# Optimization experiments

Hardware: AMD Instinct MI355X
Metric: run time of the kernel (lower is better)

## Reference

```python
import jax, jax.numpy as jnp
import numpy as np

B, Nx, Ny = 4, 4096, 8192
M1M, M2M = 8, 8            # modes1, modes2
WID = 32                   # width
HX, HY = 64, 64            # latent grid
DIN, DOUT = 1, 1
S = 16                     # n_subdomains
G = HX * HY
EPS = 1e-6

def _cplx(w):
    return w[..., 0] + 1j * w[..., 1]

def setup_inputs():
    key = jax.random.key(0)
    ks = jax.random.split(key, 20)
    rng = np.random.default_rng(0)
    ind = np.stack([rng.permutation(Ny) for _ in range(B)]).astype(np.int32)
    sep = np.tile(np.arange(S + 1) * (Ny // S), (B, 1)).astype(np.int32)
    d = {}
    d['x'] = jax.random.normal(ks[0], (B, Nx, DIN), jnp.float32)
    d['loc'] = jax.random.uniform(ks[1], (B, Ny, 2), jnp.float32)
    d['ind'] = jnp.asarray(ind)
    d['sep'] = jnp.asarray(sep)
    def lin(k, o, i):
        s = 1.0 / np.sqrt(i)
        return jax.random.uniform(k, (o, i), jnp.float32, -s, s)
    d['W_embed1'] = lin(ks[2], G, Nx); d['b_embed1'] = jnp.zeros((G,), jnp.float32)
    d['W_embed2'] = lin(ks[3], G, Ny); d['b_embed2'] = jnp.zeros((G,), jnp.float32)
    d['W_fc0'] = lin(ks[4], WID, DIN + 2); d['b_fc0'] = jnp.zeros((WID,), jnp.float32)
    sc = 1.0 / (WID * WID)
    d['conv_w1'] = sc * jax.random.uniform(ks[5], (4, WID, WID, M1M, M2M, 2), jnp.float32)
    d['conv_w2'] = sc * jax.random.uniform(ks[6], (4, WID, WID, M1M, M2M, 2), jnp.float32)
    d['wpt'] = jax.random.normal(ks[7], (4, WID, WID), jnp.float32) / np.sqrt(WID)
    d['wpt_b'] = jnp.zeros((4, WID), jnp.float32)
    scn = 1.0 / (WID * S * DOUT)
    d['nu_w1'] = scn * jax.random.uniform(ks[8], (WID, S * DOUT, 2 * M1M + 1, M2M, 2), jnp.float32)
    d['nu_w2'] = scn * jax.random.uniform(ks[9], (WID, S * DOUT, M1M + 1, 1, 2), jnp.float32)
    scw = 1.0 / (S * DOUT)
    d['nu_w'] = scw * jax.random.uniform(ks[10], (S, DOUT), jnp.float32)
    d['nu_b'] = scw * jax.random.uniform(ks[11], (S, DOUT), jnp.float32)
    d['W_de3'] = lin(ks[12], Ny, G); d['b_de3'] = jnp.zeros((Ny,), jnp.float32)
    d['W_fc1'] = lin(ks[13], 128, WID); d['b_fc1'] = jnp.zeros((128,), jnp.float32)
    d['W_fc2'] = lin(ks[14], DOUT, 128); d['b_fc2'] = jnp.zeros((DOUT,), jnp.float32)
    return d

def _spectral_conv(x, w1, w2):
    Bc, C, H, W = x.shape
    xf = jnp.fft.rfft2(x)  # (B,C,H,W//2+1)
    of = jnp.zeros((Bc, w1.shape[1], H, W // 2 + 1), dtype=xf.dtype)
    of = of.at[:, :, :M1M, :M2M].set(jnp.einsum('bixy,ioxy->boxy', xf[:, :, :M1M, :M2M], w1))
    of = of.at[:, :, -M1M:, :M2M].set(jnp.einsum('bixy,ioxy->boxy', xf[:, :, -M1M:, :M2M], w2))
    return jnp.fft.irfft2(of, s=(H, W))

def _nu_spectral_conv(x, loc, ind, sep, nu_w1, nu_w2, nu_w, nu_b):
    Bc, C, H, W = x.shape
    Nyl = loc.shape[1]
    m1, m2 = M1M, M2M
    P1, P2 = 2 * m1 + 1, 2 * m2 + 1
    # centered FFT, padded to odd size (torch: fft2 with s=[H+1-H%2, W+1-W%2], ortho)
    ft = jnp.fft.fftshift(jnp.fft.fft2(x, s=(H + 1 - H % 2, W + 1 - W % 2), norm='ortho'), axes=(-2, -1))
    o1, o2 = ft.shape[-2] // 2, ft.shape[-1] // 2
    im1 = jnp.einsum('bixy,ioxy->boxy', ft[:, :, o1 - m1:o1 + m1 + 1, o2 - m2:o2], nu_w1)  # (B,S*O,P1,m2)
    im2 = jnp.einsum('bixy,ioxy->boxy', ft[:, :, o1 - m1:o1 + 1, o2:o2 + 1], nu_w2)[..., 0]  # (B,S*O,m1+1)
    # hermitian-symmetric image assembly (same fill order as torch code)
    images = jnp.zeros((Bc, S * DOUT, P1, P2), dtype=im1.dtype)
    images = images.at[:, :, :, :m2].set(im1)
    images = images.at[:, :, :, m2 + 1:].set(jnp.flip(im1, (-1, -2)).conj())
    col = jnp.zeros((Bc, S * DOUT, P1), dtype=im1.dtype)
    col = col.at[:, :, m1:].set(jnp.flip(im2, -1).conj())
    col = col.at[:, :, :m1 + 1].set(im2)
    col = col.at[:, :, m1].set(col[:, :, m1].real.astype(im1.dtype))
    images = images.at[:, :, :, m2].set(col).reshape(Bc, S, DOUT, P1, P2)
    # per-point subdomain id: invert (ind, sep) CSR layout
    pos_sub = jax.vmap(lambda s: jnp.searchsorted(s, jnp.arange(Nyl), side='right') - 1)(sep)
    seg = jnp.zeros((Bc, Nyl), jnp.int32).at[jnp.arange(Bc)[:, None], ind].set(pos_sub.astype(jnp.int32))
    ids = (jnp.arange(Bc)[:, None] * S + seg).reshape(-1)
    locf = loc.reshape(Bc * Nyl, 2)
    mn = jax.ops.segment_min(locf, ids, num_segments=Bc * S)[ids]
    mx = jax.ops.segment_max(locf, ids, num_segments=Bc * S)[ids]
    om = (((locf - mn) / (mx - mn + EPS)) * (2 * jnp.pi) - jnp.pi).reshape(Bc, Nyl, 2)
    # exact type-2 NUDFT (torchkbnufft convention: centered grid, ortho norm;
    # module does conj(nufft(conj(images))) => positive-sign exponent)
    n1 = jnp.arange(P1) - m1
    n2 = jnp.arange(P2) - m2
    E = jnp.exp(1j * (om[..., 0, None, None] * n1[:, None] + om[..., 1, None, None] * n2[None, :]))  # (B,Ny,P1,P2)
    vals = jnp.einsum('bsoxy,bpxy->bpso', images, E).real / np.sqrt(P1 * P2)  # (B,Ny,S,O)
    vals = jnp.take_along_axis(vals, seg[:, :, None, None], axis=2)[:, :, 0, :]  # (B,Ny,O)
    out = vals * nu_w[seg] + nu_b[seg]
    return out.transpose(0, 2, 1)  # (B,O,Ny)

def _forward(x, loc, W_embed1, b_embed1, W_embed2, b_embed2, W_fc0, b_fc0,
             conv_w1, conv_w2, wpt, wpt_b, nu_w1, nu_w2, nu_w, nu_b,
             W_de3, b_de3, W_fc1, b_fc1, W_fc2, b_fc2, ind, sep):
    Bc = x.shape[0]
    xe = jnp.einsum('bnd,gn->bgd', x, W_embed1) + b_embed1[None, :, None]
    le = jnp.einsum('bnc,gn->bgc', loc, W_embed2) + b_embed2[None, :, None]
    h = jnp.concatenate([xe, le], axis=-1).reshape(Bc, HX, HY, DIN + 2)
    h = (h @ W_fc0.T + b_fc0).transpose(0, 3, 1, 2)  # (B,width,HX,HY)
    for l in range(4):
        h1 = _spectral_conv(h, _cplx(conv_w1[l]), _cplx(conv_w2[l]))
        h2 = jnp.einsum('oc,bchw->bohw', wpt[l], h) + wpt_b[l][None, :, None, None]
        h = h1 + h2
        if l < 3:
            h = jax.nn.gelu(h, approximate=False)
    x_nu = _nu_spectral_conv(h, loc, ind, sep, _cplx(nu_w1), _cplx(nu_w2), nu_w, nu_b)  # (B,O,Ny)
    hl = h.transpose(0, 2, 3, 1)
    hl = jax.nn.gelu(hl @ W_fc1.T + b_fc1, approximate=False)
    hl = hl @ W_fc2.T + b_fc2                      # (B,HX,HY,O)
    hl = hl.reshape(Bc, G, DOUT).transpose(0, 2, 1)  # (B,O,G)
    hl = hl @ W_de3.T + b_de3                       # (B,O,Ny)
    return (hl + x_nu).transpose(0, 2, 1)           # (B,Ny,O)

def reference(x, loc, ind, sep, W_embed1, b_embed1, W_embed2, b_embed2, W_fc0, b_fc0,
              conv_w1, conv_w2, wpt, wpt_b, nu_w1, nu_w2, nu_w, nu_b,
              W_de3, b_de3, W_fc1, b_fc1, W_fc2, b_fc2):
    return _forward(x, loc, W_embed1, b_embed1, W_embed2, b_embed2, W_fc0, b_fc0,
                    conv_w1, conv_w2, wpt, wpt_b, nu_w1, nu_w2, nu_w, nu_b,
                    W_de3, b_de3, W_fc1, b_fc1, W_fc2, b_fc2, ind, sep)
```

## Files before the change

### kernel.cpp

```cpp
#include <hip/hip_runtime.h>
#include <math.h>

#define BB 4
#define NX 4096
#define NYP 8192
#define GG 4096
#define WIDTH 32
#define SS 16
#define PI_F 3.14159265358979323846f

__device__ __forceinline__ float gelu_exact(float v) {
    return 0.5f * v * (1.0f + erff(v * 0.70710678118654752f));
}

__global__ __launch_bounds__(256, 2) void k_embed(
    const float* __restrict__ x, const float* __restrict__ loc,
    const float* __restrict__ We1, const float* __restrict__ be1,
    const float* __restrict__ We2, const float* __restrict__ be2,
    const float* __restrict__ Wfc0, const float* __restrict__ bfc0,
    float* __restrict__ h0)
{
    int gbase = blockIdx.x * 8;
    int t = threadIdx.x;

    float accx[32];
    #pragma unroll
    for (int k = 0; k < 32; ++k) accx[k] = 0.f;
    for (int n4 = t; n4 < NX / 4; n4 += 256) {
        float4 xb[4];
        #pragma unroll
        for (int b = 0; b < 4; ++b)
            xb[b] = ((const float4*)(x + (size_t)b * NX))[n4];
        float4 w[8];
        #pragma unroll
        for (int r = 0; r < 8; ++r)
            w[r] = ((const float4*)(We1 + (size_t)(gbase + r) * NX))[n4];
        #pragma unroll
        for (int r = 0; r < 8; ++r)
            #pragma unroll
            for (int b = 0; b < 4; ++b)
                accx[r * 4 + b] += w[r].x * xb[b].x + w[r].y * xb[b].y
                                 + w[r].z * xb[b].z + w[r].w * xb[b].w;
    }

    float accl[64];
    #pragma unroll
    for (int k = 0; k < 64; ++k) accl[k] = 0.f;
    for (int n4 = t; n4 < NYP / 4; n4 += 256) {
        float4 p0[4], p1[4];
        #pragma unroll
        for (int b = 0; b < 4; ++b) {
            const float4* lb = (const float4*)(loc + (size_t)b * NYP * 2);
            p0[b] = lb[n4 * 2];
            p1[b] = lb[n4 * 2 + 1];
        }
        float4 w[8];
        #pragma unroll
        for (int r = 0; r < 8; ++r)
            w[r] = ((const float4*)(We2 + (size_t)(gbase + r) * NYP))[n4];
        #pragma unroll
        for (int r = 0; r < 8; ++r)
            #pragma unroll
            for (int b = 0; b < 4; ++b) {
                accl[r * 4 + b]      += w[r].x * p0[b].x + w[r].y * p0[b].z
                                      + w[r].z * p1[b].x + w[r].w * p1[b].z;
                accl[32 + r * 4 + b] += w[r].x * p0[b].y + w[r].y * p0[b].w
                                      + w[r].z * p1[b].y + w[r].w * p1[b].w;
            }
    }

    #pragma unroll
    for (int k = 0; k < 32; ++k)
        for (int off = 32; off > 0; off >>= 1) accx[k] += __shfl_down(accx[k], off);
    #pragma unroll
    for (int k = 0; k < 64; ++k)
        for (int off = 32; off > 0; off >>= 1) accl[k] += __shfl_down(accl[k], off);
    __shared__ float red[4][96];
    __shared__ float tot[96];
    int wave = t >> 6, lane = t & 63;
    if (lane == 0) {
        for (int k = 0; k < 32; ++k) red[wave][k] = accx[k];
        for (int k = 0; k < 64; ++k) red[wave][32 + k] = accl[k];
    }
    __syncthreads();
    if (t < 96) tot[t] = red[0][t] + red[1][t] + red[2][t] + red[3][t];
    __syncthreads();
    if (t < 128) {
        int b = t >> 5, w = t & 31;
        float w0 = Wfc0[w * 3 + 0], w1c = Wfc0[w * 3 + 1], w2c = Wfc0[w * 3 + 2], bb0 = bfc0[w];
        #pragma unroll
        for (int r = 0; r < 8; ++r) {
            int g = gbase + r;
            float xe = tot[r * 4 + b] + be1[g];
            float l0 = tot[32 + r * 4 + b] + be2[g];
            float l1 = tot[64 + r * 4 + b] + be2[g];
            h0[((size_t)(b * WIDTH + w)) * GG + g] = xe * w0 + l0 * w1c + l1 * w2c + bb0;
        }
    }
}

__global__ __launch_bounds__(256) void k_xf(const float* __restrict__ h, float* __restrict__ xf)
{
    int bc = blockIdx.x;
    int t = threadIdx.x;
    __shared__ float sh[64 * 66];
    __shared__ float twc[8 * 64], tws[8 * 64];
    __shared__ float s1[64 * 8 * 2];
    const float* hp = h + (size_t)bc * 4096;
    for (int i = t; i < 4096; i += 256) sh[(i >> 6) * 66 + (i & 63)] = hp[i];
    for (int i = t; i < 512; i += 256) {
        int ky = i >> 6, y = i & 63;
        float s, c;
        sincosf(-2.f * PI_F * (float)(ky * y) / 64.f, &s, &c);
        twc[i] = c; tws[i] = s;
    }
    __syncthreads();
    for (int task = t; task < 512; task += 256) {
        int xx = task >> 3, ky = task & 7;
        float sr = 0.f, si = 0.f;
        const float* row = sh + xx * 66;
        const float* tc = twc + ky * 64;
        const float* ts = tws + ky * 64;
        for (int y = 0; y < 64; ++y) { sr += row[y] * tc[y]; si += row[y] * ts[y]; }
        s1[(xx * 8 + ky) * 2 + 0] = sr;
        s1[(xx * 8 + ky) * 2 + 1] = si;
    }
    __syncthreads();
    if (t < 128) {
        int kxi = t >> 3, ky = t & 7;
        int kx = (kxi < 8) ? kxi : (kxi - 16);
        float ar = 0.f, ai = 0.f;
        for (int xx = 0; xx < 64; ++xx) {
            float s, c;
            sincosf(-2.f * PI_F * (float)(kx * xx) / 64.f, &s, &c);
            float vr = s1[(xx * 8 + ky) * 2], vi = s1[(xx * 8 + ky) * 2 + 1];
            ar += vr * c - vi * s;
            ai += vr * s + vi * c;
        }
        xf[((size_t)bc * 128 + t) * 2 + 0] = ar;
        xf[((size_t)bc * 128 + t) * 2 + 1] = ai;
    }
}

__global__ __launch_bounds__(256) void k_mix(
    const float* __restrict__ xf,
    const float* __restrict__ w1, const float* __restrict__ w2,
    float* __restrict__ stt)
{
    int blk = blockIdx.x;
    int b = blk >> 5, o = blk & 31;
    int t = threadIdx.x;
    __shared__ float sxf[32 * 128 * 2];
    __shared__ float sof[128 * 2];
    __shared__ float cxc[16 * 64], cxs[16 * 64];
    const float* xfb = xf + (size_t)b * 32 * 128 * 2;
    for (int i = t; i < 32 * 128 * 2; i += 256) sxf[i] = xfb[i];
    for (int i = t; i < 1024; i += 256) {
        int kxi = i >> 6, xx = i & 63;
        int kx = (kxi < 8) ? kxi : (kxi - 16);
        float s, c;
        sincosf(2.f * PI_F * (float)(kx * xx) / 64.f, &s, &c);
        cxc[i] = c; cxs[i] = s;
    }
    __syncthreads();
    if (t < 128) {
        int kxi = t >> 3, ky = t & 7;
        const float* w = (kxi < 8) ? w1 : w2;
        int kxw = kxi & 7;
        float ar = 0.f, ai = 0.f;
        for (int i = 0; i < 32; ++i) {
            size_t wi0 = (((size_t)(i * 32 + o) * 8 + kxw) * 8 + ky) * 2;
            float wr = w[wi0], wimag = w[wi0 + 1];
            float xr = sxf[(i * 128 + t) * 2], xi = sxf[(i * 128 + t) * 2 + 1];
            ar += xr * wr - xi * wimag;
            ai += xr * wimag + xi * wr;
        }
        sof[t * 2 + 0] = ar; sof[t * 2 + 1] = ai;
    }
    __syncthreads();
    for (int task = t; task < 512; task += 256) {
        int xx = task >> 3, ky = task & 7;
        float ar = 0.f, ai = 0.f;
        #pragma unroll
        for (int kxi = 0; kxi < 16; ++kxi) {
            float c = cxc[kxi * 64 + xx], s = cxs[kxi * 64 + xx];
            float vr = sof[(kxi * 8 + ky) * 2], vi = sof[(kxi * 8 + ky) * 2 + 1];
            ar += vr * c - vi * s;
            ai += vr * s + vi * c;
        }
        stt[(size_t)blk * 1024 + (xx * 8 + ky) * 2 + 0] = ar * (1.f / 64.f);
        stt[(size_t)blk * 1024 + (xx * 8 + ky) * 2 + 1] = ai * (1.f / 64.f);
    }
}

__global__ __launch_bounds__(256) void k_pw(
    const float* __restrict__ h, const float* __restrict__ stt,
    const float* __restrict__ wpt, const float* __restrict__ wptb,
    float* __restrict__ hout, int do_gelu)
{
    int blk = blockIdx.x;
    int b = blk >> 6, xx = blk & 63;
    int t = threadIdx.x;
    __shared__ float sh[32 * 64];
    __shared__ float sst[32 * 16];
    __shared__ float swp[32 * 32];
    __shared__ float swb[32];
    __shared__ float cy[8 * 64], sy[8 * 64];
    for (int i = t; i < 2048; i += 256) {
        int c = i >> 6, y = i & 63;
        sh[i] = h[((size_t)(b * 32 + c)) * 4096 + xx * 64 + y];
    }
    for (int i = t; i < 512; i += 256) {
        int o = i >> 4, r = i & 15;
        sst[i] = stt[((size_t)(b * 32 + o)) * 1024 + xx * 16 + r];
    }
    for (int i = t; i < 1024; i += 256) swp[i] = wpt[i];
    if (t < 32) swb[t] = wptb[t];
    for (int i = t; i < 512; i += 256) {
        int ky = i >> 6, y = i & 63;
        float s, c;
        sincosf(2.f * PI_F * (float)(ky * y) / 64.f, &s, &c);
        cy[i] = c; sy[i] = s;
    }
    __syncthreads();
    int o = t >> 3, y0 = t & 7;
    float wb = swb[o];
    #pragma unroll
    for (int k = 0; k < 8; ++k) {
        int y = y0 + 8 * k;
        float sp = sst[o * 16 + 0];
        #pragma unroll
        for (int ky = 1; ky < 8; ++ky)
            sp += 2.f * (sst[o * 16 + ky * 2]     * cy[ky * 64 + y]
                       - sst[o * 16 + ky * 2 + 1] * sy[ky * 64 + y]);
        sp *= (1.f / 64.f);
        float pw = wb;
        #pragma unroll
        for (int c = 0; c < 32; ++c)
            pw += swp[o * 32 + c] * sh[c * 64 + y];
        float v = sp + pw;
        if (do_gelu) v = gelu_exact(v);
        hout[((size_t)(b * 32 + o)) * 4096 + xx * 64 + y] = v;
    }
}

__global__ __launch_bounds__(256) void k_nu_fm(const float* __restrict__ h, float* __restrict__ Fm)
{
    int bc = blockIdx.x;
    int t = threadIdx.x;
    __shared__ float sh[64 * 66];
    __shared__ float twc[9 * 64], tws[9 * 64];
    __shared__ float s1[64 * 9 * 2];
    const float* hp = h + (size_t)bc * 4096;
    for (int i = t; i < 4096; i += 256) sh[(i >> 6) * 66 + (i & 63)] = hp[i];
    for (int i = t; i < 9 * 64; i += 256) {
        int bbi = i >> 6, y = i & 63;
        float s, c;
        sincosf(-2.f * PI_F * (float)((bbi - 8) * y) / 65.f, &s, &c);
        twc[i] = c; tws[i] = s;
    }
    __syncthreads();
    for (int task = t; task < 64 * 9; task += 256) {
        int xx = task / 9, bbi = task % 9;
        float sr = 0.f, si = 0.f;
        const float* row = sh + xx * 66;
        const float* tc = twc + bbi * 64;
        const float* ts = tws + bbi * 64;
        for (int y = 0; y < 64; ++y) { sr += row[y] * tc[y]; si += row[y] * ts[y]; }
        s1[(xx * 9 + bbi) * 2 + 0] = sr;
        s1[(xx * 9 + bbi) * 2 + 1] = si;
    }
    __syncthreads();
    for (int task = t; task < 17 * 9; task += 256) {
        int ai2 = task / 9, bbi = task % 9;
        int afreq = ai2 - 8;
        float ar = 0.f, aim = 0.f;
        for (int xx = 0; xx < 64; ++xx) {
            float s, c;
            sincosf(-2.f * PI_F * (float)(afreq * xx) / 65.f, &s, &c);
            float vr = s1[(xx * 9 + bbi) * 2], vi = s1[(xx * 9 + bbi) * 2 + 1];
            ar += vr * c - vi * s;
            aim += vr * s + vi * c;
        }
        Fm[((size_t)bc * 153 + task) * 2 + 0] = ar * (1.f / 65.f);
        Fm[((size_t)bc * 153 + task) * 2 + 1] = aim * (1.f / 65.f);
    }
}

__global__ __launch_bounds__(256) void k_nu_img(
    const float* __restrict__ Fm, const float* __restrict__ nw1, const float* __restrict__ nw2,
    float* __restrict__ images)
{
    int blk = blockIdx.x;
    int b = blk >> 4, s = blk & 15;
    int t = threadIdx.x;
    __shared__ float im1[17 * 8 * 2];
    __shared__ float im2[9 * 2];
    if (t < 136) {
        int xx = t >> 3, y = t & 7;
        float ar = 0.f, ai = 0.f;
        for (int i = 0; i < 32; ++i) {
            size_t f0 = (((size_t)(b * 32 + i)) * 153 + xx * 9 + y) * 2;
            size_t w0 = (((size_t)(i * 16 + s) * 17 + xx) * 8 + y) * 2;
            float fr = Fm[f0], fi = Fm[f0 + 1];
            float wr = nw1[w0], wi = nw1[w0 + 1];
            ar += fr * wr - fi * wi;
            ai += fr * wi + fi * wr;
        }
        im1[t * 2] = ar; im1[t * 2 + 1] = ai;
    } else if (t < 145) {
        int k = t - 136;
        float ar = 0.f, ai = 0.f;
        for (int i = 0; i < 32; ++i) {
            size_t f0 = (((size_t)(b * 32 + i)) * 153 + k * 9 + 8) * 2;
            size_t w0 = ((size_t)(i * 16 + s) * 9 + k) * 2;
            float fr = Fm[f0], fi = Fm[f0 + 1];
            float wr = nw2[w0], wi = nw2[w0 + 1];
            ar += fr * wr - fi * wi;
            ai += fr * wi + fi * wr;
        }
        im2[k * 2] = ar; im2[k * 2 + 1] = ai;
    }
    __syncthreads();
    for (int task = t; task < 289; task += 256) {
        int xx = task / 17, y = task % 17;
        float vr, vi;
        if (y < 8)      { vr = im1[(xx * 8 + y) * 2];            vi = im1[(xx * 8 + y) * 2 + 1]; }
        else if (y > 8) { int sx = 16 - xx, sy2 = 16 - y;
                          vr = im1[(sx * 8 + sy2) * 2];          vi = -im1[(sx * 8 + sy2) * 2 + 1]; }
        else {
            if (xx < 8)       { vr = im2[xx * 2];        vi = im2[xx * 2 + 1]; }
            else if (xx == 8) { vr = im2[16];            vi = 0.f; }
            else              { vr = im2[(16 - xx) * 2]; vi = -im2[(16 - xx) * 2 + 1]; }
        }
        images[((size_t)blk * 289 + task) * 2 + 0] = vr;
        images[((size_t)blk * 289 + task) * 2 + 1] = vi;
    }
}

__global__ __launch_bounds__(256) void k_seg(
    const int* __restrict__ ind, const int* __restrict__ sep, const float* __restrict__ loc,
    float* __restrict__ mnmx)
{
    int blk = blockIdx.x;
    int b = blk >> 4, s = blk & 15;
    int t = threadIdx.x;
    int j0 = sep[b * 17 + s], j1 = sep[b * 17 + s + 1];
    float mn0 = 1e30f, mn1 = 1e30f, mx0 = -1e30f, mx1 = -1e30f;
    for (int j = j0 + t; j < j1; j += 256) {
        int p = ind[b * NYP + j];
        float l0 = loc[((size_t)b * NYP + p) * 2];
        float l1 = loc[((size_t)b * NYP + p) * 2 + 1];
        mn0 = fminf(mn0, l0); mx0 = fmaxf(mx0, l0);
        mn1 = fminf(mn1, l1); mx1 = fmaxf(mx1, l1);
    }
    __shared__ float r[4][256];
    r[0][t] = mn0; r[1][t] = mn1; r[2][t] = mx0; r[3][t] = mx1;
    __syncthreads();
    for (int st = 128; st > 0; st >>= 1) {
        if (t < st) {
            r[0][t] = fminf(r[0][t], r[0][t + st]);
            r[1][t] = fminf(r[1][t], r[1][t + st]);
            r[2][t] = fmaxf(r[2][t], r[2][t + st]);
            r[3][t] = fmaxf(r[3][t], r[3][t + st]);
        }
        __syncthreads();
    }
    if (t == 0) {
        mnmx[blk * 4 + 0] = r[0][0]; mnmx[blk * 4 + 1] = r[1][0];
        mnmx[blk * 4 + 2] = r[2][0]; mnmx[blk * 4 + 3] = r[3][0];
    }
}

__global__ __launch_bounds__(256) void k_nudft(
    const int* __restrict__ ind, const int* __restrict__ sep, const float* __restrict__ loc,
    const float* __restrict__ images, const float* __restrict__ mnmx,
    const float* __restrict__ nu_w, const float* __restrict__ nu_b,
    float* __restrict__ xnu)
{
    int blk = blockIdx.x;
    int b = blk >> 4, s = blk & 15;
    int t = threadIdx.x;
    __shared__ float img[289 * 2];
    for (int i = t; i < 578; i += 256) img[i] = images[(size_t)blk * 578 + i];
    __syncthreads();
    int j0 = sep[b * 17 + s], j1 = sep[b * 17 + s + 1];
    float mn0 = mnmx[blk * 4], mn1 = mnmx[blk * 4 + 1];
    float mx0 = mnmx[blk * 4 + 2], mx1 = mnmx[blk * 4 + 3];
    float nuw = nu_w[s], nub = nu_b[s];
    const float TWO_PI = 6.28318530717958647692f;
    for (int j = j0 + t; j < j1; j += 256) {
        int p = ind[b * NYP + j];
        float l0 = loc[((size_t)b * NYP + p) * 2];
        float l1 = loc[((size_t)b * NYP + p) * 2 + 1];
        float om0 = (l0 - mn0) / (mx0 - mn0 + 1e-6f) * TWO_PI - PI_F;
        float om1 = (l1 - mn1) / (mx1 - mn1 + 1e-6f) * TWO_PI - PI_F;
        float stepxs, stepxc, stepys, stepyc;
        sincosf(om0, &stepxs, &stepxc);
        sincosf(om1, &stepys, &stepyc);
        float ex_i, ex_r, ey0_i, ey0_r;
        sincosf(-8.f * om0, &ex_i, &ex_r);
        sincosf(-8.f * om1, &ey0_i, &ey0_r);
        float tot = 0.f;
        for (int xx = 0; xx < 17; ++xx) {
            float inr = 0.f, ini = 0.f;
            float eyr = ey0_r, eyi = ey0_i;
            const float* row = img + xx * 34;
            #pragma unroll
            for (int y = 0; y < 17; ++y) {
                float ir = row[y * 2], ii = row[y * 2 + 1];
                inr += ir * eyr - ii * eyi;
                ini += ir * eyi + ii * eyr;
                float nr = eyr * stepyc - eyi * stepys;
                eyi = eyr * stepys + eyi * stepyc;
                eyr = nr;
            }
            tot += ex_r * inr - ex_i * ini;
            float nr = ex_r * stepxc - ex_i * stepxs;
            ex_i = ex_r * stepxs + ex_i * stepxc;
            ex_r = nr;
        }
        xnu[(size_t)b * NYP + p] = (tot * (1.f / 17.f)) * nuw + nub;
    }
}

__global__ __launch_bounds__(256) void k_head(
    const float* __restrict__ h, const float* __restrict__ Wfc1, const float* __restrict__ bfc1,
    const float* __restrict__ Wfc2, const float* __restrict__ bfc2, float* __restrict__ q)
{
    __shared__ float w1s[128 * 32];
    __shared__ float b1s[128];
    __shared__ float w2s[128];
    int t = threadIdx.x;
    for (int i = t; i < 4096; i += 256) w1s[i] = Wfc1[i];
    if (t < 128) { b1s[t] = bfc1[t]; w2s[t] = Wfc2[t]; }
    __syncthreads();
    int id = blockIdx.x * 256 + t;
    int b = id >> 12, g = id & 4095;
    float hv[32];
    #pragma unroll
    for (int c = 0; c < 32; ++c) hv[c] = h[((size_t)(b * 32 + c)) * GG + g];
    float acc = bfc2[0];
    for (int j = 0; j < 128; ++j) {
        float z = b1s[j];
        #pragma unroll
        for (int c = 0; c < 32; ++c) z += w1s[j * 32 + c] * hv[c];
        acc += w2s[j] * gelu_exact(z);
    }
    q[id] = acc;
}

__global__ __launch_bounds__(256) void k_de3(
    const float* __restrict__ Wde3, const float* __restrict__ bde3,
    const float* __restrict__ q, const float* __restrict__ xnu, float* __restrict__ out)
{
    int nbase = blockIdx.x * 8;
    int t = threadIdx.x;
    float acc[32];
    #pragma unroll
    for (int k = 0; k < 32; ++k) acc[k] = 0.f;
    for (int g4 = t; g4 < GG / 4; g4 += 256) {
        float4 qb[4];
        #pragma unroll
        for (int b = 0; b < 4; ++b)
            qb[b] = ((const float4*)(q + (size_t)b * GG))[g4];
        float4 w[8];
        #pragma unroll
        for (int r = 0; r < 8; ++r)
            w[r] = ((const float4*)(Wde3 + (size_t)(nbase + r) * GG))[g4];
        #pragma unroll
        for (int r = 0; r < 8; ++r)
            #pragma unroll
            for (int b = 0; b < 4; ++b)
                acc[r * 4 + b] += w[r].x * qb[b].x + w[r].y * qb[b].y
                                + w[r].z * qb[b].z + w[r].w * qb[b].w;
    }
    #pragma unroll
    for (int k = 0; k < 32; ++k)
        for (int off = 32; off > 0; off >>= 1) acc[k] += __shfl_down(acc[k], off);
    __shared__ float red[4][32];
    int wave = t >> 6, lane = t & 63;
    if (lane == 0)
        for (int k = 0; k < 32; ++k) red[wave][k] = acc[k];
    __syncthreads();
    if (t < 32) {
        float v = red[0][t] + red[1][t] + red[2][t] + red[3][t];
        int r = t >> 2, b = t & 3;
        int n = nbase + r;
        out[(size_t)b * NYP + n] = v + bde3[n] + xnu[(size_t)b * NYP + n];
    }
}

extern "C" void kernel_launch(void* const* d_in, const int* in_sizes, int n_in,
                              void* d_out, int out_size, void* d_ws, size_t ws_size,
                              hipStream_t stream) {
    const float* x    = (const float*)d_in[0];
    const float* loc  = (const float*)d_in[1];
    const int*   ind  = (const int*)d_in[2];
    const int*   sep  = (const int*)d_in[3];
    const float* We1  = (const float*)d_in[4];
    const float* be1  = (const float*)d_in[5];
    const float* We2  = (const float*)d_in[6];
    const float* be2  = (const float*)d_in[7];
    const float* Wfc0 = (const float*)d_in[8];
    const float* bfc0 = (const float*)d_in[9];
    const float* cw1  = (const float*)d_in[10];
    const float* cw2  = (const float*)d_in[11];
    const float* wpt  = (const float*)d_in[12];
    const float* wptb = (const float*)d_in[13];
    const float* nw1  = (const float*)d_in[14];
    const float* nw2  = (const float*)d_in[15];
    const float* nuw  = (const float*)d_in[16];
    const float* nub  = (const float*)d_in[17];
    const float* Wde3 = (const float*)d_in[18];
    const float* bde3 = (const float*)d_in[19];
    const float* Wfc1 = (const float*)d_in[20];
    const float* bfc1 = (const float*)d_in[21];
    const float* Wfc2 = (const float*)d_in[22];
    const float* bfc2 = (const float*)d_in[23];
    float* out = (float*)d_out;

    float* ws     = (float*)d_ws;
    float* hA     = ws;
    float* hB     = hA + (size_t)BB * WIDTH * GG;
    float* xfbuf  = hB + (size_t)BB * WIDTH * GG;
    float* Fm     = xfbuf + (size_t)BB * WIDTH * 128 * 2;
    float* images = Fm + (size_t)BB * WIDTH * 153 * 2;
    float* mnmx   = images + (size_t)BB * SS * 289 * 2;
    float* q      = mnmx + 256;
    float* xnu    = q + (size_t)BB * GG;
    float* sttbuf = xnu + (size_t)BB * NYP;

    k_seg<<<BB * SS, 256, 0, stream>>>(ind, sep, loc, mnmx);
    k_embed<<<GG / 8, 256, 0, stream>>>(x, loc, We1, be1, We2, be2, Wfc0, bfc0, hA);

    const float* hin = hA;
    float* hout = hB;
    for (int l = 0; l < 4; ++l) {
        k_xf<<<BB * WIDTH, 256, 0, stream>>>(hin, xfbuf);
        k_mix<<<BB * WIDTH, 256, 0, stream>>>(xfbuf,
                                              cw1 + (size_t)l * 16384, cw2 + (size_t)l * 16384,
                                              sttbuf);
        k_pw<<<BB * 64, 256, 0, stream>>>(hin, sttbuf, wpt + l * 1024, wptb + l * 32,
                                          hout, (l < 3) ? 1 : 0);
        float* tmp = (float*)hin; hin = hout; hout = tmp;
    }
    k_nu_fm<<<BB * WIDTH, 256, 0, stream>>>(hin, Fm);
    k_nu_img<<<BB * SS, 256, 0, stream>>>(Fm, nw1, nw2, images);
    k_nudft<<<BB * SS, 256, 0, stream>>>(ind, sep, loc, images, mnmx, nuw, nub, xnu);
    k_head<<<(BB * GG) / 256, 256, 0, stream>>>(hin, Wfc1, bfc1, Wfc2, bfc2, q);
    k_de3<<<NYP / 8, 256, 0, stream>>>(Wde3, bde3, q, xnu, out);
}
```

Measured before the change: 600.4 us.

## Replace inner-loop sincos with twiddle tables, stage mix weights, fuse segment minmax

The per-iteration sincosf calls in the second DFT pass of k_xf and k_nu_fm are replaced with shared-memory twiddle tables indexed by a modular phase counter. k_mix stages its slice of the spectral weights into shared memory and unrolls the channel loop, replacing strided global reads. The k_seg min/max kernel is folded into k_nudft, which removes one launch and the mnmx round-trip through global memory. In exchange, shared memory per block grows, and each nudft block now scans its segment's locations twice.

```diff
diff --git a/kernel.cpp b/kernel.cpp
--- a/kernel.cpp
+++ b/kernel.cpp
@@ -105,6 +105,7 @@
     int t = threadIdx.x;
     __shared__ float sh[64 * 66];
     __shared__ float twc[8 * 64], tws[8 * 64];
+    __shared__ float tb64c[64], tb64s[64];
     __shared__ float s1[64 * 8 * 2];
     const float* hp = h + (size_t)bc * 4096;
     for (int i = t; i < 4096; i += 256) sh[(i >> 6) * 66 + (i & 63)] = hp[i];
@@ -113,6 +114,11 @@
         float s, c;
         sincosf(-2.f * PI_F * (float)(ky * y) / 64.f, &s, &c);
         twc[i] = c; tws[i] = s;
+    }
+    if (t < 64) {
+        float s, c;
+        sincosf(-2.f * PI_F * (float)t / 64.f, &s, &c);
+        tb64c[t] = c; tb64s[t] = s;
     }
     __syncthreads();
     for (int task = t; task < 512; task += 256) {
@@ -130,12 +136,13 @@
         int kxi = t >> 3, ky = t & 7;
         int kx = (kxi < 8) ? kxi : (kxi - 16);
         float ar = 0.f, ai = 0.f;
+        int m = 0;
         for (int xx = 0; xx < 64; ++xx) {
-            float s, c;
-            sincosf(-2.f * PI_F * (float)(kx * xx) / 64.f, &s, &c);
+            float c = tb64c[m], s = tb64s[m];
             float vr = s1[(xx * 8 + ky) * 2], vi = s1[(xx * 8 + ky) * 2 + 1];
             ar += vr * c - vi * s;
             ai += vr * s + vi * c;
+            m = (m + kx) & 63;
         }
         xf[((size_t)bc * 128 + t) * 2 + 0] = ar;
         xf[((size_t)bc * 128 + t) * 2 + 1] = ai;
@@ -153,8 +160,14 @@
     __shared__ float sxf[32 * 128 * 2];
     __shared__ float sof[128 * 2];
     __shared__ float cxc[16 * 64], cxs[16 * 64];
+    __shared__ float sw1[32 * 128], sw2[32 * 128];
     const float* xfb = xf + (size_t)b * 32 * 128 * 2;
     for (int i = t; i < 32 * 128 * 2; i += 256) sxf[i] = xfb[i];
+    for (int i = t; i < 32 * 128; i += 256) {
+        int ii = i >> 7, e = i & 127;
+        sw1[i] = w1[((size_t)(ii * 32 + o)) * 128 + e];
+        sw2[i] = w2[((size_t)(ii * 32 + o)) * 128 + e];
+    }
     for (int i = t; i < 1024; i += 256) {
         int kxi = i >> 6, xx = i & 63;
         int kx = (kxi < 8) ? kxi : (kxi - 16);
@@ -165,12 +178,13 @@
     __syncthreads();
     if (t < 128) {
         int kxi = t >> 3, ky = t & 7;
-        const float* w = (kxi < 8) ? w1 : w2;
+        const float* w = (kxi < 8) ? sw1 : sw2;
         int kxw = kxi & 7;
+        int e = (kxw * 8 + ky) * 2;
         float ar = 0.f, ai = 0.f;
+        #pragma unroll
         for (int i = 0; i < 32; ++i) {
-            size_t wi0 = (((size_t)(i * 32 + o) * 8 + kxw) * 8 + ky) * 2;
-            float wr = w[wi0], wimag = w[wi0 + 1];
+            float wr = w[i * 128 + e], wimag = w[i * 128 + e + 1];
             float xr = sxf[(i * 128 + t) * 2], xi = sxf[(i * 128 + t) * 2 + 1];
             ar += xr * wr - xi * wimag;
             ai += xr * wimag + xi * wr;
@@ -250,6 +264,7 @@
     int t = threadIdx.x;
     __shared__ float sh[64 * 66];
     __shared__ float twc[9 * 64], tws[9 * 64];
+    __shared__ float t65c[65], t65s[65];
     __shared__ float s1[64 * 9 * 2];
     const float* hp = h + (size_t)bc * 4096;
     for (int i = t; i < 4096; i += 256) sh[(i >> 6) * 66 + (i & 63)] = hp[i];
@@ -258,6 +273,11 @@
         float s, c;
         sincosf(-2.f * PI_F * (float)((bbi - 8) * y) / 65.f, &s, &c);
         twc[i] = c; tws[i] = s;
+    }
+    if (t < 65) {
+        float s, c;
+        sincosf(-2.f * PI_F * (float)t / 65.f, &s, &c);
+        t65c[t] = c; t65s[t] = s;
     }
     __syncthreads();
     for (int task = t; task < 64 * 9; task += 256) {
@@ -275,12 +295,15 @@
         int ai2 = task / 9, bbi = task % 9;
         int afreq = ai2 - 8;
         float ar = 0.f, aim = 0.f;
+        int m = 0;
         for (int xx = 0; xx < 64; ++xx) {
-            float s, c;
-            sincosf(-2.f * PI_F * (float)(afreq * xx) / 65.f, &s, &c);
+            float c = t65c[m], s = t65s[m];
             float vr = s1[(xx * 9 + bbi) * 2], vi = s1[(xx * 9 + bbi) * 2 + 1];
             ar += vr * c - vi * s;
             aim += vr * s + vi * c;
+            m += afreq;
+            if (m < 0) m += 65;
+            else if (m >= 65) m -= 65;
         }
         Fm[((size_t)bc * 153 + task) * 2 + 0] = ar * (1.f / 65.f);
         Fm[((size_t)bc * 153 + task) * 2 + 1] = aim * (1.f / 65.f);
@@ -338,13 +361,18 @@
     }
 }
 
-__global__ __launch_bounds__(256) void k_seg(
+__global__ __launch_bounds__(256) void k_nudft(
     const int* __restrict__ ind, const int* __restrict__ sep, const float* __restrict__ loc,
-    float* __restrict__ mnmx)
+    const float* __restrict__ images,
+    const float* __restrict__ nu_w, const float* __restrict__ nu_b,
+    float* __restrict__ xnu)
 {
     int blk = blockIdx.x;
     int b = blk >> 4, s = blk & 15;
     int t = threadIdx.x;
+    __shared__ float img[289 * 2];
+    __shared__ float r[4][256];
+    for (int i = t; i < 578; i += 256) img[i] = images[(size_t)blk * 578 + i];
     int j0 = sep[b * 17 + s], j1 = sep[b * 17 + s + 1];
     float mn0 = 1e30f, mn1 = 1e30f, mx0 = -1e30f, mx1 = -1e30f;
     for (int j = j0 + t; j < j1; j += 256) {
@@ -354,7 +382,6 @@
         mn0 = fminf(mn0, l0); mx0 = fmaxf(mx0, l0);
         mn1 = fminf(mn1, l1); mx1 = fmaxf(mx1, l1);
     }
-    __shared__ float r[4][256];
     r[0][t] = mn0; r[1][t] = mn1; r[2][t] = mx0; r[3][t] = mx1;
     __syncthreads();
     for (int st = 128; st > 0; st >>= 1) {
@@ -366,27 +393,7 @@
         }
         __syncthreads();
     }
-    if (t == 0) {
-        mnmx[blk * 4 + 0] = r[0][0]; mnmx[blk * 4 + 1] = r[1][0];
-        mnmx[blk * 4 + 2] = r[2][0]; mnmx[blk * 4 + 3] = r[3][0];
-    }
-}
-
-__global__ __launch_bounds__(256) void k_nudft(
-    const int* __restrict__ ind, const int* __restrict__ sep, const float* __restrict__ loc,
-    const float* __restrict__ images, const float* __restrict__ mnmx,
-    const float* __restrict__ nu_w, const float* __restrict__ nu_b,
-    float* __restrict__ xnu)
-{
-    int blk = blockIdx.x;
-    int b = blk >> 4, s = blk & 15;
-    int t = threadIdx.x;
-    __shared__ float img[289 * 2];
-    for (int i = t; i < 578; i += 256) img[i] = images[(size_t)blk * 578 + i];
-    __syncthreads();
-    int j0 = sep[b * 17 + s], j1 = sep[b * 17 + s + 1];
-    float mn0 = mnmx[blk * 4], mn1 = mnmx[blk * 4 + 1];
-    float mx0 = mnmx[blk * 4 + 2], mx1 = mnmx[blk * 4 + 3];
+    mn0 = r[0][0]; mn1 = r[1][0]; mx0 = r[2][0]; mx1 = r[3][0];
     float nuw = nu_w[s], nub = nu_b[s];
     const float TWO_PI = 6.28318530717958647692f;
     for (int j = j0 + t; j < j1; j += 256) {
@@ -531,7 +538,6 @@
     float* xnu    = q + (size_t)BB * GG;
     float* sttbuf = xnu + (size_t)BB * NYP;
 
-    k_seg<<<BB * SS, 256, 0, stream>>>(ind, sep, loc, mnmx);
     k_embed<<<GG / 8, 256, 0, stream>>>(x, loc, We1, be1, We2, be2, Wfc0, bfc0, hA);
 
     const float* hin = hA;
@@ -547,7 +553,7 @@
     }
     k_nu_fm<<<BB * WIDTH, 256, 0, stream>>>(hin, Fm);
     k_nu_img<<<BB * SS, 256, 0, stream>>>(Fm, nw1, nw2, images);
-    k_nudft<<<BB * SS, 256, 0, stream>>>(ind, sep, loc, images, mnmx, nuw, nub, xnu);
+    k_nudft<<<BB * SS, 256, 0, stream>>>(ind, sep, loc, images, nuw, nub, xnu);
     k_head<<<(BB * GG) / 256, 256, 0, stream>>>(hin, Wfc1, bfc1, Wfc2, bfc2, q);
     k_de3<<<NYP / 8, 256, 0, stream>>>(Wde3, bde3, q, xnu, out);
 }
```

Measured after the change: 571.6 us. 1.05x faster.
